# Kernel tuning notes

Hardware: AMD Instinct MI355X
Metric: run time of the kernel (lower is better)

The kernel has to match this reference:

```python
import jax, jax.numpy as jnp
import numpy as np

HEADS = 8
DIM_HEAD = 128
ATTN_MATRIX_SCALE = 1.5  # tau applied to mean-centered logits
SCALE = DIM_HEAD ** -0.5


def setup_inputs() -> dict:
    key = jax.random.key(0)
    ks = jax.random.split(key, 7)
    b, n, m = 2, 2048, 2048
    qd, cd, inner = 1024, 768, HEADS * DIM_HEAD
    x = jax.random.normal(ks[0], (b, n, qd), dtype=jnp.float32)
    context = jax.random.normal(ks[1], (b, m, cd), dtype=jnp.float32)
    Wq = jax.random.normal(ks[2], (qd, inner), dtype=jnp.float32) * (qd ** -0.5)
    Wk = jax.random.normal(ks[3], (cd, inner), dtype=jnp.float32) * (cd ** -0.5)
    Wv = jax.random.normal(ks[4], (cd, inner), dtype=jnp.float32) * (cd ** -0.5)
    Wout = jax.random.normal(ks[5], (inner, qd), dtype=jnp.float32) * (inner ** -0.5)
    bout = jnp.zeros((qd,), dtype=jnp.float32)
    return {"x": x, "context": context, "Wq": Wq, "Wk": Wk, "Wv": Wv,
            "Wout": Wout, "bout": bout}


def _split_heads(t):
    # (b, n, h*d) -> (h, b*n, d); matches rearrange '(b h) n d -> h (b n) d'
    b, n, _ = t.shape
    t = t.reshape(b, n, HEADS, DIM_HEAD)
    return t.transpose(2, 0, 1, 3).reshape(HEADS, b * n, DIM_HEAD)


def reference(x, context, Wq, Wk, Wv, Wout, bout):
    b, n, _ = x.shape
    qh = _split_heads(jnp.einsum('bnq,qi->bni', x, Wq))        # (h, b*n, d)
    kh = _split_heads(jnp.einsum('bmc,ci->bmi', context, Wk))  # (h, b*m, d)
    vh = _split_heads(jnp.einsum('bmc,ci->bmi', context, Wv))  # (h, b*m, d)

    # custom mean-centered / tau-scaled similarity (_compute_sim_with_tau)
    sim = jnp.einsum('hid,hjd->hij', qh, kh) * SCALE
    mean = jnp.mean(sim, axis=-1, keepdims=True)
    sim = (sim - mean) * ATTN_MATRIX_SCALE + mean

    attn = jax.nn.softmax(sim, axis=-1)
    out = jnp.einsum('hij,hjd->hid', attn, vh)                 # (h, b*n, d)

    # (h, b*n, d) -> (b, n, h*d)
    out = out.reshape(HEADS, b, n, DIM_HEAD).transpose(1, 2, 0, 3)
    out = out.reshape(b, n, HEADS * DIM_HEAD)
    return jnp.einsum('bni,iq->bnq', out, Wout) + bout
```

## Files before the change

kernel.cpp:

```cpp
#include <hip/hip_runtime.h>
#include <cstdint>
#include <cstddef>

typedef unsigned short u16t;
typedef __bf16 bf16x8_t __attribute__((ext_vector_type(8)));
typedef float f32x4_t __attribute__((ext_vector_type(4)));

#define MFMA_BF16 __builtin_amdgcn_mfma_f32_16x16x32_bf16

__device__ __forceinline__ u16t f2bf(float f) {
    uint32_t u = __builtin_bit_cast(uint32_t, f);
    u += 0x7fffu + ((u >> 16) & 1u);
    return (u16t)(u >> 16);
}

__device__ __forceinline__ uint32_t pk2bf(float a, float b) {
    return (uint32_t)f2bf(a) | ((uint32_t)f2bf(b) << 16);
}

__device__ __forceinline__ bf16x8_t ld_frag(const u16t* p) {
    return __builtin_bit_cast(bf16x8_t, *(const uint4*)p);
}

__device__ __forceinline__ void gl_lds16(const u16t* g, u16t* l) {
    __builtin_amdgcn_global_load_lds(
        (const __attribute__((address_space(1))) void*)g,
        (__attribute__((address_space(3))) void*)l, 16, 0, 0);
}

__global__ void cast_bf16_kernel(const float* __restrict__ src, u16t* __restrict__ dst, int n4) {
    int i = blockIdx.x * blockDim.x + threadIdx.x;
    if (i >= n4) return;
    float4 v = ((const float4*)src)[i];
    uint2 o;
    o.x = pk2bf(v.x, v.y);
    o.y = pk2bf(v.z, v.w);
    ((uint2*)dst)[i] = o;
}

__global__ void transpose_cast_kernel(const float* __restrict__ W, u16t* __restrict__ Wt,
                                      int K, int N) {
    __shared__ float tile[32][33];
    int n0 = blockIdx.x * 32, k0 = blockIdx.y * 32;
    int tx = threadIdx.x, ty = threadIdx.y;
    for (int i = ty; i < 32; i += 8)
        tile[i][tx] = W[(size_t)(k0 + i) * N + n0 + tx];
    __syncthreads();
    for (int i = ty; i < 32; i += 8)
        Wt[(size_t)(n0 + i) * K + k0 + tx] = f2bf(tile[tx][i]);
}

__global__ __launch_bounds__(256) void gemm_bf16_kernel(
    const u16t* __restrict__ A, const u16t* __restrict__ Bt,
    int K, void* __restrict__ outp, const float* __restrict__ bias,
    int mode, float oscale)
{
    __shared__ __align__(16) u16t As[128 * 64];
    __shared__ __align__(16) u16t Bs[64 * 64];
    const int bm = blockIdx.y * 128, bn = blockIdx.x * 64;
    const int tid = threadIdx.x;
    const int wave = tid >> 6, lane = tid & 63;
    const int wm = wave & 1, wn = wave >> 1;
    const int quad = lane >> 4, l16 = lane & 15;

    f32x4_t acc[4][2];
#pragma unroll
    for (int i = 0; i < 4; ++i)
#pragma unroll
        for (int j = 0; j < 2; ++j) acc[i][j] = (f32x4_t){0.f, 0.f, 0.f, 0.f};

    for (int kc = 0; kc < K; kc += 64) {
        __syncthreads();
#pragma unroll
        for (int it = 0; it < 4; ++it) {
            int r = (tid >> 3) + it * 32;
            int c8 = tid & 7;
            uint4 va = *(const uint4*)&A[(size_t)(bm + r) * K + kc + c8 * 8];
            *(uint4*)&As[r * 64 + ((c8 ^ (r & 7)) * 8)] = va;
        }
#pragma unroll
        for (int it = 0; it < 2; ++it) {
            int r = (tid >> 3) + it * 32;
            int c8 = tid & 7;
            uint4 vb = *(const uint4*)&Bt[(size_t)(bn + r) * K + kc + c8 * 8];
            *(uint4*)&Bs[r * 64 + ((c8 ^ (r & 7)) * 8)] = vb;
        }
        __syncthreads();
#pragma unroll
        for (int ks = 0; ks < 2; ++ks) {
            bf16x8_t af[4], bfv[2];
#pragma unroll
            for (int i = 0; i < 4; ++i) {
                int r = wm * 64 + i * 16 + l16;
                af[i] = ld_frag(&As[r * 64 + (((ks * 4 + quad) ^ (r & 7)) * 8)]);
            }
#pragma unroll
            for (int j = 0; j < 2; ++j) {
                int r = wn * 32 + j * 16 + l16;
                bfv[j] = ld_frag(&Bs[r * 64 + (((ks * 4 + quad) ^ (r & 7)) * 8)]);
            }
#pragma unroll
            for (int i = 0; i < 4; ++i)
#pragma unroll
                for (int j = 0; j < 2; ++j)
                    acc[i][j] = MFMA_BF16(af[i], bfv[j], acc[i][j], 0, 0, 0);
        }
    }

    if (mode == 3) {
        float* out = (float*)outp;
#pragma unroll
        for (int j = 0; j < 2; ++j) {
            int c = bn + wn * 32 + j * 16 + l16;
            float b = bias[c];
#pragma unroll
            for (int i = 0; i < 4; ++i) {
                int rb = bm + wm * 64 + i * 16 + quad * 4;
#pragma unroll
                for (int r = 0; r < 4; ++r)
                    out[(size_t)(rb + r) * 1024 + c] = acc[i][j][r] + b;
            }
        }
    } else if (mode == 2) {
        u16t* out = (u16t*)outp;
#pragma unroll
        for (int i = 0; i < 4; ++i)
#pragma unroll
            for (int j = 0; j < 2; ++j) {
                int rb = bm + wm * 64 + i * 16 + quad * 4;
                int c = bn + wn * 32 + j * 16 + l16;
                int h = c >> 7, d = c & 127;
                uint2 pk;
                pk.x = pk2bf(acc[i][j][0], acc[i][j][1]);
                pk.y = pk2bf(acc[i][j][2], acc[i][j][3]);
                *(uint2*)&out[((size_t)h * 128 + d) * 4096 + rb] = pk;
            }
    } else {
        u16t* out = (u16t*)outp;
#pragma unroll
        for (int i = 0; i < 4; ++i)
#pragma unroll
            for (int j = 0; j < 2; ++j) {
                int rb = bm + wm * 64 + i * 16 + quad * 4;
                int c = bn + wn * 32 + j * 16 + l16;
                int h = c >> 7, d = c & 127;
#pragma unroll
                for (int r = 0; r < 4; ++r)
                    out[((size_t)h * 4096 + rb + r) * 128 + d] = f2bf(acc[i][j][r] * oscale);
            }
    }
}

__global__ __launch_bounds__(256) void flash_kernel(
    const u16t* __restrict__ Qh, const u16t* __restrict__ Kh,
    const u16t* __restrict__ Vtg, u16t* __restrict__ Oh)
{
    extern __shared__ __align__(16) u16t smem[];
    u16t* Ps = smem + 32768;

    const int h = blockIdx.x;
    const int q0 = blockIdx.y * 64;
    const int tid = threadIdx.x;
    const int wave = tid >> 6, lane = tid & 63;
    const int quad = lane >> 4, l16 = lane & 15;

    const u16t* Kg = Kh + (size_t)h * 4096 * 128;
    const u16t* Vg = Vtg + (size_t)h * 128 * 4096;

    {
        const u16t* Qg = Qh + ((size_t)h * 4096 + q0) * 128;
        const int sr = tid >> 4, c8 = tid & 15;
#pragma unroll
        for (int it = 0; it < 4; ++it) {
            int r = sr + it * 16;
            uint4 v = *(const uint4*)&Qg[r * 128 + c8 * 8];
            *(uint4*)&smem[r * 128 + ((c8 ^ (r & 15)) * 8)] = v;
        }
    }
    __syncthreads();
    bf16x8_t qf[4];
    {
        int r = wave * 16 + l16;
#pragma unroll
        for (int ks = 0; ks < 4; ++ks)
            qf[ks] = ld_frag(&smem[r * 128 + (((ks * 4 + quad) ^ (r & 15)) * 8)]);
    }
    __syncthreads();

    const int rK = lane >> 4, cK = lane & 15;
    const int rV = lane >> 3, cV = lane & 7;

#pragma unroll
    for (int it = 0; it < 4; ++it) {
        int r = wave * 16 + it * 4 + rK;
        gl_lds16(Kg + (size_t)r * 128 + (cK ^ (r & 15)) * 8,
                 smem + (wave * 16 + it * 4) * 128);
        int rv = wave * 32 + it * 8 + rV;
        gl_lds16(Vg + (size_t)rv * 4096 + (cV ^ (rv & 7)) * 8,
                 smem + 16384 + (wave * 32 + it * 8) * 64);
    }

    f32x4_t O[8];
#pragma unroll
    for (int dt = 0; dt < 8; ++dt) O[dt] = (f32x4_t){0.f, 0.f, 0.f, 0.f};
    float lsum = 0.f;
    const int prow = wave * 16 + l16;

    for (int kb = 0; kb < 64; ++kb) {
        const int bo  = (kb & 1) * 8192;
        const int bon = 8192 - bo;
        __syncthreads();

        if (kb < 63) {
            const int j0n = (kb + 1) * 64;
#pragma unroll
            for (int it = 0; it < 4; ++it) {
                int r = wave * 16 + it * 4 + rK;
                gl_lds16(Kg + ((size_t)(j0n + r)) * 128 + (cK ^ (r & 15)) * 8,
                         smem + bon + (wave * 16 + it * 4) * 128);
                int rv = wave * 32 + it * 8 + rV;
                gl_lds16(Vg + (size_t)rv * 4096 + j0n + (cV ^ (rv & 7)) * 8,
                         smem + 16384 + bon + (wave * 32 + it * 8) * 64);
            }
        }

        const u16t* Ks = smem + bo;
        const u16t* Vs = smem + 16384 + bo;

        f32x4_t S[4];
#pragma unroll
        for (int jt = 0; jt < 4; ++jt) {
            S[jt] = (f32x4_t){0.f, 0.f, 0.f, 0.f};
            int rk = jt * 16 + l16;
#pragma unroll
            for (int ks = 0; ks < 4; ++ks) {
                bf16x8_t kf = ld_frag(&Ks[rk * 128 + (((ks * 4 + quad) ^ (rk & 15)) * 8)]);
                S[jt] = MFMA_BF16(kf, qf[ks], S[jt], 0, 0, 0);
            }
        }

#pragma unroll
        for (int jt = 0; jt < 4; ++jt) {
            float e0 = __builtin_amdgcn_exp2f(S[jt][0]);
            float e1 = __builtin_amdgcn_exp2f(S[jt][1]);
            float e2 = __builtin_amdgcn_exp2f(S[jt][2]);
            float e3 = __builtin_amdgcn_exp2f(S[jt][3]);
            lsum += (e0 + e1) + (e2 + e3);
            uint2 pk;
            pk.x = pk2bf(e0, e1);
            pk.y = pk2bf(e2, e3);
            int ch = (jt * 2 + (quad >> 1)) ^ (prow & 7);
            *(uint2*)&Ps[prow * 64 + ch * 8 + (quad & 1) * 4] = pk;
        }

#pragma unroll
        for (int ks2 = 0; ks2 < 2; ++ks2) {
            bf16x8_t pf = ld_frag(&Ps[prow * 64 + (((ks2 * 4 + quad) ^ (prow & 7)) * 8)]);
#pragma unroll
            for (int dt = 0; dt < 8; ++dt) {
                int rv = dt * 16 + l16;
                bf16x8_t vf = ld_frag(&Vs[rv * 64 + (((ks2 * 4 + quad) ^ (rv & 7)) * 8)]);
                O[dt] = MFMA_BF16(vf, pf, O[dt], 0, 0, 0);
            }
        }
    }

    lsum += __shfl_xor(lsum, 16, 64);
    lsum += __shfl_xor(lsum, 32, 64);
    float inv = 1.f / lsum;
    size_t i = (size_t)(q0 + wave * 16 + l16);
#pragma unroll
    for (int dt = 0; dt < 8; ++dt) {
        uint2 pk;
        pk.x = pk2bf(O[dt][0] * inv, O[dt][1] * inv);
        pk.y = pk2bf(O[dt][2] * inv, O[dt][3] * inv);
        *(uint2*)&Oh[i * 1024 + h * 128 + dt * 16 + quad * 4] = pk;
    }
}

extern "C" void kernel_launch(void* const* d_in, const int* in_sizes, int n_in,
                              void* d_out, int out_size, void* d_ws, size_t ws_size,
                              hipStream_t stream)
{
    (void)in_sizes; (void)n_in; (void)out_size; (void)ws_size;
    const float* x    = (const float*)d_in[0];
    const float* ctx  = (const float*)d_in[1];
    const float* Wq   = (const float*)d_in[2];
    const float* Wk   = (const float*)d_in[3];
    const float* Wv   = (const float*)d_in[4];
    const float* Wout = (const float*)d_in[5];
    const float* bout = (const float*)d_in[6];
    float* out = (float*)d_out;

    u16t* ws = (u16t*)d_ws;
    u16t* x_bf   = ws;
    u16t* ctx_bf = x_bf + 4194304;
    u16t* Wqt    = ctx_bf + 3145728;
    u16t* Wkt    = Wqt + 1048576;
    u16t* Wvt    = Wkt + 786432;
    u16t* Woutt  = Wvt + 786432;
    u16t* Qh     = Woutt + 1048576;
    u16t* Kh     = Qh + 4194304;
    u16t* Vt     = Kh + 4194304;
    u16t* Oh     = x_bf;

    constexpr float QSCALE = 1.5f * 0.08838834764831845f * 1.4426950408889634f;

    (void)hipFuncSetAttribute((const void*)flash_kernel,
                              hipFuncAttributeMaxDynamicSharedMemorySize, 73728);

    cast_bf16_kernel<<<4096, 256, 0, stream>>>(x, x_bf, 1048576);
    cast_bf16_kernel<<<3072, 256, 0, stream>>>(ctx, ctx_bf, 786432);
    transpose_cast_kernel<<<dim3(32, 32), dim3(32, 8), 0, stream>>>(Wq, Wqt, 1024, 1024);
    transpose_cast_kernel<<<dim3(32, 24), dim3(32, 8), 0, stream>>>(Wk, Wkt, 768, 1024);
    transpose_cast_kernel<<<dim3(32, 24), dim3(32, 8), 0, stream>>>(Wv, Wvt, 768, 1024);
    transpose_cast_kernel<<<dim3(32, 32), dim3(32, 8), 0, stream>>>(Wout, Woutt, 1024, 1024);

    gemm_bf16_kernel<<<dim3(16, 32), 256, 0, stream>>>(x_bf,   Wqt, 1024, Qh, nullptr, 0, QSCALE);
    gemm_bf16_kernel<<<dim3(16, 32), 256, 0, stream>>>(ctx_bf, Wkt,  768, Kh, nullptr, 0, 1.0f);
    gemm_bf16_kernel<<<dim3(16, 32), 256, 0, stream>>>(ctx_bf, Wvt,  768, Vt, nullptr, 2, 1.0f);

    flash_kernel<<<dim3(8, 64), 256, 73728, stream>>>(Qh, Kh, Vt, Oh);

    gemm_bf16_kernel<<<dim3(16, 32), 256, 0, stream>>>(Oh, Woutt, 1024, out, bout, 3, 1.0f);
}
```

Before: 285.1 us.

## Double-buffer GEMM shared tiles with direct global-to-LDS prefetch

New measurement: 275.7 us. -3.3%, faster.

```diff
diff --git a/kernel.cpp b/kernel.cpp
--- a/kernel.cpp
+++ b/kernel.cpp
@@ -55,49 +55,66 @@
     int K, void* __restrict__ outp, const float* __restrict__ bias,
     int mode, float oscale)
 {
-    __shared__ __align__(16) u16t As[128 * 64];
-    __shared__ __align__(16) u16t Bs[64 * 64];
+    __shared__ __align__(16) u16t As[2][128 * 64];
+    __shared__ __align__(16) u16t Bs[2][64 * 64];
     const int bm = blockIdx.y * 128, bn = blockIdx.x * 64;
     const int tid = threadIdx.x;
     const int wave = tid >> 6, lane = tid & 63;
     const int wm = wave & 1, wn = wave >> 1;
     const int quad = lane >> 4, l16 = lane & 15;
 
+    const int l8r = lane >> 3, l8c = lane & 7;
+    const int cgx = (l8c ^ l8r) * 8;
+
     f32x4_t acc[4][2];
 #pragma unroll
     for (int i = 0; i < 4; ++i)
 #pragma unroll
         for (int j = 0; j < 2; ++j) acc[i][j] = (f32x4_t){0.f, 0.f, 0.f, 0.f};
 
-    for (int kc = 0; kc < K; kc += 64) {
+    const int nk = K >> 6;
+
+#pragma unroll
+    for (int it = 0; it < 4; ++it) {
+        int rb = wave * 32 + it * 8;
+        gl_lds16(&A[(size_t)(bm + rb + l8r) * K + cgx], &As[0][rb * 64]);
+    }
+#pragma unroll
+    for (int it = 0; it < 2; ++it) {
+        int rb = wave * 16 + it * 8;
+        gl_lds16(&Bt[(size_t)(bn + rb + l8r) * K + cgx], &Bs[0][rb * 64]);
+    }
+
+    for (int ki = 0; ki < nk; ++ki) {
+        const int buf = ki & 1;
         __syncthreads();
-#pragma unroll
-        for (int it = 0; it < 4; ++it) {
-            int r = (tid >> 3) + it * 32;
-            int c8 = tid & 7;
-            uint4 va = *(const uint4*)&A[(size_t)(bm + r) * K + kc + c8 * 8];
-            *(uint4*)&As[r * 64 + ((c8 ^ (r & 7)) * 8)] = va;
-        }
-#pragma unroll
-        for (int it = 0; it < 2; ++it) {
-            int r = (tid >> 3) + it * 32;
-            int c8 = tid & 7;
-            uint4 vb = *(const uint4*)&Bt[(size_t)(bn + r) * K + kc + c8 * 8];
-            *(uint4*)&Bs[r * 64 + ((c8 ^ (r & 7)) * 8)] = vb;
-        }
-        __syncthreads();
+
+        if (ki + 1 < nk) {
+            const int kc = (ki + 1) << 6;
+#pragma unroll
+            for (int it = 0; it < 4; ++it) {
+                int rb = wave * 32 + it * 8;
+                gl_lds16(&A[(size_t)(bm + rb + l8r) * K + kc + cgx], &As[buf ^ 1][rb * 64]);
+            }
+#pragma unroll
+            for (int it = 0; it < 2; ++it) {
+                int rb = wave * 16 + it * 8;
+                gl_lds16(&Bt[(size_t)(bn + rb + l8r) * K + kc + cgx], &Bs[buf ^ 1][rb * 64]);
+            }
+        }
+
 #pragma unroll
         for (int ks = 0; ks < 2; ++ks) {
             bf16x8_t af[4], bfv[2];
 #pragma unroll
             for (int i = 0; i < 4; ++i) {
                 int r = wm * 64 + i * 16 + l16;
-                af[i] = ld_frag(&As[r * 64 + (((ks * 4 + quad) ^ (r & 7)) * 8)]);
+                af[i] = ld_frag(&As[buf][r * 64 + (((ks * 4 + quad) ^ (r & 7)) * 8)]);
             }
 #pragma unroll
             for (int j = 0; j < 2; ++j) {
                 int r = wn * 32 + j * 16 + l16;
-                bfv[j] = ld_frag(&Bs[r * 64 + (((ks * 4 + quad) ^ (r & 7)) * 8)]);
+                bfv[j] = ld_frag(&Bs[buf][r * 64 + (((ks * 4 + quad) ^ (r & 7)) * 8)]);
             }
 #pragma unroll
             for (int i = 0; i < 4; ++i)
```
